# Performance work log

Measured on AMD Instinct MI355X. Metric: run time of the kernel, lower is better.

## Reference

```python
import jax, jax.numpy as jnp
import numpy as np

D_MODEL, D_FF, N_EXPERTS, TOP_K = 1024, 4096, 8, 2

def setup_inputs() -> dict:
    key = jax.random.key(0)
    k0, k1, k2, k3 = jax.random.split(key, 4)
    x = jax.random.normal(k0, (2, 2048, D_MODEL), dtype=jnp.float32)
    Wg = jax.random.normal(k1, (D_MODEL, N_EXPERTS), dtype=jnp.float32) * 0.02
    W1 = jax.random.normal(k2, (N_EXPERTS, D_MODEL, D_FF), dtype=jnp.float32) * 0.02
    b1 = jnp.zeros((N_EXPERTS, D_FF), dtype=jnp.float32)
    W2 = jax.random.normal(k3, (N_EXPERTS, D_FF, D_MODEL), dtype=jnp.float32) * 0.02
    b2 = jnp.zeros((N_EXPERTS, D_MODEL), dtype=jnp.float32)
    return {"x": x, "Wg": Wg, "W1": W1, "b1": b1, "W2": W2, "b2": b2}

def reference(x, Wg, W1, b1, W2, b2):
    B = x.shape[:-1]
    xs = x.reshape(-1, x.shape[-1])                 # [T, D]
    T = xs.shape[0]
    gate_logits = xs @ Wg                           # [T, E]
    weights, sel = jax.lax.top_k(gate_logits, TOP_K)  # [T, k]
    # softmax over the top-k logits, computed in fp32 then cast back (matches F.softmax(dtype=float).type_as)
    weights = jax.nn.softmax(weights.astype(jnp.float32), axis=1).astype(x.dtype)
    # dense all-experts MLP: [E, T, D_FF] -> [E, T, D]
    h = jax.nn.relu(jnp.einsum('td,edf->etf', xs, W1) + b1[:, None, :])
    out_e = jnp.einsum('etf,efd->etd', h, W2) + b2[:, None, :]
    # gather each token's top-k expert outputs and combine with routing weights
    tok = jnp.arange(T)
    picked = out_e[sel, tok[:, None]]               # [T, k, D]
    out = jnp.einsum('tk,tkd->td', weights, picked) # [T, D]
    return out.reshape(*B, x.shape[-1])
```

## Files before the change

### kernel.cpp

```cpp
#include <hip/hip_runtime.h>
#include <cstdint>
#include <cstddef>

#define T_TOKENS 4096
#define DM 1024
#define DF 4096
#define NE 8
#define TOPK 2
#define BK 32
#define MAX_MT 72

typedef short short8 __attribute__((ext_vector_type(8)));
typedef float f32x4 __attribute__((ext_vector_type(4)));

__device__ __forceinline__ unsigned short f2h_bits(float f) {
  _Float16 h = (_Float16)f;
  union { _Float16 h; unsigned short u; } v; v.h = h; return v.u;
}

typedef __attribute__((address_space(3))) void lds_void_t;
typedef __attribute__((address_space(1))) void gvoid_t;
__device__ __forceinline__ void gl_lds16(const void* g, void* l) {
  __builtin_amdgcn_global_load_lds((gvoid_t*)g, (lds_void_t*)l, 16, 0, 0);
}

__global__ void gate_kernel(const float* __restrict__ x, const float* __restrict__ Wg,
                            int* __restrict__ sel, float* __restrict__ wts,
                            int* __restrict__ counts) {
  int wave = threadIdx.x >> 6, lane = threadIdx.x & 63;
  int t = blockIdx.x * 4 + wave;
  const float* xr = x + (size_t)t * DM;
  float acc[NE];
#pragma unroll
  for (int e = 0; e < NE; e++) acc[e] = 0.f;
#pragma unroll
  for (int j = 0; j < DM / 64; j++) {
    int d = lane + 64 * j;
    float xv = xr[d];
    const float* wr = Wg + (size_t)d * NE;
#pragma unroll
    for (int e = 0; e < NE; e++) acc[e] += xv * wr[e];
  }
#pragma unroll
  for (int e = 0; e < NE; e++) {
    float v = acc[e];
#pragma unroll
    for (int off = 32; off > 0; off >>= 1) v += __shfl_down(v, off, 64);
    acc[e] = v;
  }
  if (lane == 0) {
    int b0 = 0;
#pragma unroll
    for (int e = 1; e < NE; e++) if (acc[e] > acc[b0]) b0 = e;
    int b1 = (b0 == 0) ? 1 : 0;
#pragma unroll
    for (int e = 0; e < NE; e++) if (e != b0 && acc[e] > acc[b1]) b1 = e;
    float p = expf(acc[b1] - acc[b0]);
    float w0 = 1.f / (1.f + p);
    sel[t * 2] = b0; sel[t * 2 + 1] = b1;
    wts[t * 2] = w0; wts[t * 2 + 1] = p * w0;
    atomicAdd(&counts[b0], 1);
    atomicAdd(&counts[b1], 1);
  }
}

__global__ void scan_kernel(const int* __restrict__ counts, int* __restrict__ offsets,
                            int* __restrict__ tile_off, int* __restrict__ cursors) {
  if (threadIdx.x == 0) {
    int o = 0, to = 0;
    offsets[0] = 0; tile_off[0] = 0;
    for (int e = 0; e < NE; e++) {
      cursors[e] = o;
      o += counts[e];
      to += (counts[e] + 127) >> 7;
      offsets[e + 1] = o;
      tile_off[e + 1] = to;
    }
  }
}

__global__ void scatter_kernel(const int* __restrict__ sel, const float* __restrict__ wts,
                               int* __restrict__ cursors, int* __restrict__ rows,
                               float* __restrict__ rw) {
  int t = blockIdx.x * 256 + threadIdx.x;
  if (t >= T_TOKENS) return;
#pragma unroll
  for (int k = 0; k < TOPK; k++) {
    int e = sel[t * 2 + k];
    int slot = atomicAdd(&cursors[e], 1);
    rows[slot] = t;
    rw[slot] = wts[t * 2 + k];
  }
}

__global__ void gather_kernel(const float* __restrict__ x, const int* __restrict__ rows,
                              unsigned short* __restrict__ Xg) {
  int wave = threadIdx.x >> 6, lane = threadIdx.x & 63;
  int s = blockIdx.x * 4 + wave;
  int t = rows[s];
  const float4* src = (const float4*)(x + (size_t)t * DM);
  ushort4* dst = (ushort4*)(Xg + (size_t)s * DM);
#pragma unroll
  for (int j = 0; j < 4; j++) {
    float4 v = src[lane + 64 * j];
    ushort4 o;
    o.x = f2h_bits(v.x); o.y = f2h_bits(v.y); o.z = f2h_bits(v.z); o.w = f2h_bits(v.w);
    dst[lane + 64 * j] = o;
  }
}

__global__ void transpose_convert(const float* __restrict__ in, unsigned short* __restrict__ outp,
                                  int R, int C) {
  __shared__ float tile[32][33];
  const float* inE = in + (size_t)blockIdx.z * R * C;
  unsigned short* outE = outp + (size_t)blockIdx.z * R * C;
  int c0 = blockIdx.x * 32, r0 = blockIdx.y * 32;
  int tx = threadIdx.x, ty = threadIdx.y;
#pragma unroll
  for (int k = 0; k < 4; k++)
    tile[ty + 8 * k][tx] = inE[(size_t)(r0 + ty + 8 * k) * C + c0 + tx];
  __syncthreads();
#pragma unroll
  for (int k = 0; k < 4; k++)
    outE[(size_t)(c0 + ty + 8 * k) * R + r0 + tx] = f2h_bits(tile[tx][ty + 8 * k]);
}

template <int K, int N, bool SECOND>
__global__ __launch_bounds__(256, 2) void moe_gemm(
    const unsigned short* __restrict__ Aall, const unsigned short* __restrict__ Ball,
    unsigned short* __restrict__ Hout, float* __restrict__ out,
    const float* __restrict__ bias, const int* __restrict__ counts,
    const int* __restrict__ offsets, const int* __restrict__ tile_off,
    const int* __restrict__ rows, const float* __restrict__ rw) {
  __shared__ __align__(16) unsigned short ldsA[128 * BK];
  __shared__ __align__(16) unsigned short ldsB[128 * BK];

  int bx = blockIdx.x;
  int e = 0;
#pragma unroll 1
  while (e < NE && bx >= tile_off[e + 1]) e++;
  if (e >= NE) return;
  int lt = bx - tile_off[e];
  int cnt = counts[e];
  int m0 = lt * 128;
  int rowbase = offsets[e];
  int n0 = blockIdx.y * 128;

  const unsigned short* Ae = Aall + (size_t)rowbase * K;
  const unsigned short* Be = Ball + ((size_t)e * N + n0) * K;

  int tid = threadIdx.x;
  int lane = tid & 63, wave = tid >> 6;
  int wm = wave & 1, wn = wave >> 1;

  int rA0 = tid >> 2, rA1 = (256 + tid) >> 2, seg = tid & 3;
  int gA0 = m0 + rA0; if (gA0 >= cnt) gA0 = cnt - 1;
  int gA1 = m0 + rA1; if (gA1 >= cnt) gA1 = cnt - 1;
  const unsigned short* srcA0 = Ae + (size_t)gA0 * K + seg * 8;
  const unsigned short* srcA1 = Ae + (size_t)gA1 * K + seg * 8;
  const unsigned short* srcB0 = Be + (size_t)rA0 * K + seg * 8;
  const unsigned short* srcB1 = Be + (size_t)rA1 * K + seg * 8;
  unsigned short* dA0 = ldsA + (size_t)tid * 8;
  unsigned short* dA1 = ldsA + (size_t)(256 + tid) * 8;
  unsigned short* dB0 = ldsB + (size_t)tid * 8;
  unsigned short* dB1 = ldsB + (size_t)(256 + tid) * 8;

  f32x4 acc[4][4] = {};

  for (int kk = 0; kk < K; kk += BK) {
    gl_lds16(srcA0 + kk, dA0);
    gl_lds16(srcA1 + kk, dA1);
    gl_lds16(srcB0 + kk, dB0);
    gl_lds16(srcB1 + kk, dB1);
    __syncthreads();

    short8 af[4], bfr[4];
#pragma unroll
    for (int t4 = 0; t4 < 4; t4++) {
      af[t4]  = *(const short8*)(ldsA + (wm * 64 + t4 * 16 + (lane & 15)) * BK + (lane >> 4) * 8);
      bfr[t4] = *(const short8*)(ldsB + (wn * 64 + t4 * 16 + (lane & 15)) * BK + (lane >> 4) * 8);
    }
#pragma unroll
    for (int tm = 0; tm < 4; tm++)
#pragma unroll
      for (int tn = 0; tn < 4; tn++)
        acc[tm][tn] = __builtin_amdgcn_mfma_f32_16x16x32_f16(af[tm], bfr[tn], acc[tm][tn], 0, 0, 0);
    __syncthreads();
  }

  int quad = lane >> 4, c16 = lane & 15;
#pragma unroll
  for (int tm = 0; tm < 4; tm++) {
#pragma unroll
    for (int tn = 0; tn < 4; tn++) {
      int gcol = n0 + wn * 64 + tn * 16 + c16;
      float b = bias[e * N + gcol];
#pragma unroll
      for (int r = 0; r < 4; r++) {
        int rl = wm * 64 + tm * 16 + quad * 4 + r;
        if (m0 + rl < cnt) {
          float v = acc[tm][tn][r] + b;
          if constexpr (!SECOND) {
            v = fmaxf(v, 0.f);
            Hout[(size_t)(rowbase + m0 + rl) * N + gcol] = f2h_bits(v);
          } else {
            int slot = rowbase + m0 + rl;
            atomicAdd(out + (size_t)rows[slot] * N + gcol, v * rw[slot]);
          }
        }
      }
    }
  }
}

extern "C" void kernel_launch(void* const* d_in, const int* in_sizes, int n_in,
                              void* d_out, int out_size, void* d_ws, size_t ws_size,
                              hipStream_t stream) {
  const float* x  = (const float*)d_in[0];
  const float* Wg = (const float*)d_in[1];
  const float* W1 = (const float*)d_in[2];
  const float* b1 = (const float*)d_in[3];
  const float* W2 = (const float*)d_in[4];
  const float* b2 = (const float*)d_in[5];
  float* out = (float*)d_out;

  char* ws = (char*)d_ws;
  int*   counts   = (int*)(ws + 0);
  int*   cursors  = (int*)(ws + 64);
  int*   offsets  = (int*)(ws + 128);
  int*   tile_off = (int*)(ws + 192);
  int*   sel      = (int*)(ws + 256);
  float* wts      = (float*)(ws + 33024);
  int*   rows     = (int*)(ws + 65792);
  float* rw       = (float*)(ws + 98560);
  unsigned short* Xg  = (unsigned short*)(ws + 131328);
  unsigned short* H   = (unsigned short*)(ws + 131328 + 16777216);
  unsigned short* W1t = (unsigned short*)(ws + 131328 + 16777216 + 67108864);
  unsigned short* W2t = (unsigned short*)(ws + 131328 + 16777216 + 2 * 67108864);

  hipMemsetAsync(ws, 0, 256, stream);
  hipMemsetAsync(d_out, 0, (size_t)out_size * sizeof(float), stream);

  gate_kernel<<<T_TOKENS / 4, 256, 0, stream>>>(x, Wg, sel, wts, counts);
  scan_kernel<<<1, 64, 0, stream>>>(counts, offsets, tile_off, cursors);
  scatter_kernel<<<T_TOKENS / 256, 256, 0, stream>>>(sel, wts, cursors, rows, rw);
  gather_kernel<<<(TOPK * T_TOKENS) / 4, 256, 0, stream>>>(x, rows, Xg);
  transpose_convert<<<dim3(DF / 32, DM / 32, NE), dim3(32, 8), 0, stream>>>(W1, W1t, DM, DF);
  transpose_convert<<<dim3(DM / 32, DF / 32, NE), dim3(32, 8), 0, stream>>>(W2, W2t, DF, DM);

  moe_gemm<DM, DF, false><<<dim3(MAX_MT, DF / 128), 256, 0, stream>>>(
      Xg, W1t, H, out, b1, counts, offsets, tile_off, rows, rw);
  moe_gemm<DF, DM, true><<<dim3(MAX_MT, DM / 128), 256, 0, stream>>>(
      H, W2t, nullptr, out, b2, counts, offsets, tile_off, rows, rw);
}
```

Before: 754.1 us.

## Replace gather and atomic combine with indirect A loads, staged stores, deterministic combine

The gate kernel now writes an fp16 copy of x, and the first GEMM reads rows through the token index, which removes the separate gather kernel. The weight transpose switches to 64x64 tiles with float4 loads and 16-byte fp16 stores. The first GEMM stages its ReLU output through LDS so H is written with wide coalesced stores. The second GEMM writes weighted per-slot results to a scratch buffer, and a new combine kernel sums each token's two slots, replacing fp32 atomics and the output memset. The cost is an extra fp32 scratch buffer, reusing the W1t region, plus one more kernel launch.

```diff
diff --git a/kernel.cpp b/kernel.cpp
--- a/kernel.cpp
+++ b/kernel.cpp
@@ -26,10 +26,11 @@
 
 __global__ void gate_kernel(const float* __restrict__ x, const float* __restrict__ Wg,
                             int* __restrict__ sel, float* __restrict__ wts,
-                            int* __restrict__ counts) {
+                            int* __restrict__ counts, unsigned short* __restrict__ Xh) {
   int wave = threadIdx.x >> 6, lane = threadIdx.x & 63;
   int t = blockIdx.x * 4 + wave;
   const float* xr = x + (size_t)t * DM;
+  unsigned short* xh = Xh + (size_t)t * DM;
   float acc[NE];
 #pragma unroll
   for (int e = 0; e < NE; e++) acc[e] = 0.f;
@@ -37,6 +38,7 @@
   for (int j = 0; j < DM / 64; j++) {
     int d = lane + 64 * j;
     float xv = xr[d];
+    xh[d] = f2h_bits(xv);
     const float* wr = Wg + (size_t)d * NE;
 #pragma unroll
     for (int e = 0; e < NE; e++) acc[e] += xv * wr[e];
@@ -81,7 +83,7 @@
 
 __global__ void scatter_kernel(const int* __restrict__ sel, const float* __restrict__ wts,
                                int* __restrict__ cursors, int* __restrict__ rows,
-                               float* __restrict__ rw) {
+                               float* __restrict__ rw, int* __restrict__ inv) {
   int t = blockIdx.x * 256 + threadIdx.x;
   if (t >= T_TOKENS) return;
 #pragma unroll
@@ -90,50 +92,47 @@
     int slot = atomicAdd(&cursors[e], 1);
     rows[slot] = t;
     rw[slot] = wts[t * 2 + k];
-  }
-}
-
-__global__ void gather_kernel(const float* __restrict__ x, const int* __restrict__ rows,
-                              unsigned short* __restrict__ Xg) {
-  int wave = threadIdx.x >> 6, lane = threadIdx.x & 63;
-  int s = blockIdx.x * 4 + wave;
-  int t = rows[s];
-  const float4* src = (const float4*)(x + (size_t)t * DM);
-  ushort4* dst = (ushort4*)(Xg + (size_t)s * DM);
-#pragma unroll
-  for (int j = 0; j < 4; j++) {
-    float4 v = src[lane + 64 * j];
-    ushort4 o;
-    o.x = f2h_bits(v.x); o.y = f2h_bits(v.y); o.z = f2h_bits(v.z); o.w = f2h_bits(v.w);
-    dst[lane + 64 * j] = o;
+    inv[t * 2 + k] = slot;
   }
 }
 
 __global__ void transpose_convert(const float* __restrict__ in, unsigned short* __restrict__ outp,
                                   int R, int C) {
-  __shared__ float tile[32][33];
+  __shared__ unsigned short ldsT[64 * 72];
   const float* inE = in + (size_t)blockIdx.z * R * C;
   unsigned short* outE = outp + (size_t)blockIdx.z * R * C;
-  int c0 = blockIdx.x * 32, r0 = blockIdx.y * 32;
-  int tx = threadIdx.x, ty = threadIdx.y;
-#pragma unroll
-  for (int k = 0; k < 4; k++)
-    tile[ty + 8 * k][tx] = inE[(size_t)(r0 + ty + 8 * k) * C + c0 + tx];
+  int c0 = blockIdx.x * 64, r0 = blockIdx.y * 64;
+  int tid = threadIdx.x;
+  int rr = tid >> 4, cc4 = (tid & 15) * 4;
+#pragma unroll
+  for (int it = 0; it < 4; it++) {
+    int r = rr + 16 * it;
+    float4 v = *(const float4*)(inE + (size_t)(r0 + r) * C + c0 + cc4);
+    ldsT[(cc4 + 0) * 72 + r] = f2h_bits(v.x);
+    ldsT[(cc4 + 1) * 72 + r] = f2h_bits(v.y);
+    ldsT[(cc4 + 2) * 72 + r] = f2h_bits(v.z);
+    ldsT[(cc4 + 3) * 72 + r] = f2h_bits(v.w);
+  }
   __syncthreads();
 #pragma unroll
-  for (int k = 0; k < 4; k++)
-    outE[(size_t)(c0 + ty + 8 * k) * R + r0 + tx] = f2h_bits(tile[tx][ty + 8 * k]);
-}
-
-template <int K, int N, bool SECOND>
+  for (int it = 0; it < 2; it++) {
+    int idx = tid + 256 * it;
+    int c = idx >> 3, r8 = (idx & 7) * 8;
+    short8 val = *(const short8*)(ldsT + c * 72 + r8);
+    *(short8*)(outE + (size_t)(c0 + c) * R + r0 + r8) = val;
+  }
+}
+
+template <int K, int N, bool INDIR, bool SECOND>
 __global__ __launch_bounds__(256, 2) void moe_gemm(
     const unsigned short* __restrict__ Aall, const unsigned short* __restrict__ Ball,
-    unsigned short* __restrict__ Hout, float* __restrict__ out,
+    unsigned short* __restrict__ Hout, float* __restrict__ Sout,
     const float* __restrict__ bias, const int* __restrict__ counts,
     const int* __restrict__ offsets, const int* __restrict__ tile_off,
     const int* __restrict__ rows, const float* __restrict__ rw) {
-  __shared__ __align__(16) unsigned short ldsA[128 * BK];
-  __shared__ __align__(16) unsigned short ldsB[128 * BK];
+  __shared__ __align__(16) unsigned short lds[8704];
+  unsigned short* ldsA = lds;
+  unsigned short* ldsB = lds + 4096;
 
   int bx = blockIdx.x;
   int e = 0;
@@ -146,7 +145,6 @@
   int rowbase = offsets[e];
   int n0 = blockIdx.y * 128;
 
-  const unsigned short* Ae = Aall + (size_t)rowbase * K;
   const unsigned short* Be = Ball + ((size_t)e * N + n0) * K;
 
   int tid = threadIdx.x;
@@ -154,10 +152,12 @@
   int wm = wave & 1, wn = wave >> 1;
 
   int rA0 = tid >> 2, rA1 = (256 + tid) >> 2, seg = tid & 3;
-  int gA0 = m0 + rA0; if (gA0 >= cnt) gA0 = cnt - 1;
-  int gA1 = m0 + rA1; if (gA1 >= cnt) gA1 = cnt - 1;
-  const unsigned short* srcA0 = Ae + (size_t)gA0 * K + seg * 8;
-  const unsigned short* srcA1 = Ae + (size_t)gA1 * K + seg * 8;
+  int mA0 = m0 + rA0; if (mA0 >= cnt) mA0 = cnt - 1;
+  int mA1 = m0 + rA1; if (mA1 >= cnt) mA1 = cnt - 1;
+  size_t ia0 = INDIR ? (size_t)rows[rowbase + mA0] : (size_t)(rowbase + mA0);
+  size_t ia1 = INDIR ? (size_t)rows[rowbase + mA1] : (size_t)(rowbase + mA1);
+  const unsigned short* srcA0 = Aall + ia0 * K + seg * 8;
+  const unsigned short* srcA1 = Aall + ia1 * K + seg * 8;
   const unsigned short* srcB0 = Be + (size_t)rA0 * K + seg * 8;
   const unsigned short* srcB1 = Be + (size_t)rA1 * K + seg * 8;
   unsigned short* dA0 = ldsA + (size_t)tid * 8;
@@ -189,27 +189,71 @@
   }
 
   int quad = lane >> 4, c16 = lane & 15;
-#pragma unroll
-  for (int tm = 0; tm < 4; tm++) {
-#pragma unroll
-    for (int tn = 0; tn < 4; tn++) {
-      int gcol = n0 + wn * 64 + tn * 16 + c16;
-      float b = bias[e * N + gcol];
-#pragma unroll
-      for (int r = 0; r < 4; r++) {
-        int rl = wm * 64 + tm * 16 + quad * 4 + r;
-        if (m0 + rl < cnt) {
-          float v = acc[tm][tn][r] + b;
-          if constexpr (!SECOND) {
-            v = fmaxf(v, 0.f);
-            Hout[(size_t)(rowbase + m0 + rl) * N + gcol] = f2h_bits(v);
-          } else {
+  if constexpr (!SECOND) {
+#pragma unroll 1
+    for (int half = 0; half < 2; half++) {
+      __syncthreads();
+      if (wm == half) {
+#pragma unroll
+        for (int tm = 0; tm < 4; tm++) {
+#pragma unroll
+          for (int tn = 0; tn < 4; tn++) {
+            int colL = wn * 64 + tn * 16 + c16;
+            float b = bias[e * N + n0 + colL];
+#pragma unroll
+            for (int r = 0; r < 4; r++) {
+              int rl = tm * 16 + quad * 4 + r;
+              float v = fmaxf(acc[tm][tn][r] + b, 0.f);
+              lds[rl * 136 + colL] = f2h_bits(v);
+            }
+          }
+        }
+      }
+      __syncthreads();
+#pragma unroll
+      for (int i = 0; i < 4; i++) {
+        int idx = tid + 256 * i;
+        int row = idx >> 4, c8 = (idx & 15) * 8;
+        int grow = m0 + half * 64 + row;
+        if (grow < cnt) {
+          short8 val = *(const short8*)(lds + row * 136 + c8);
+          *(short8*)(Hout + (size_t)(rowbase + grow) * N + n0 + c8) = val;
+        }
+      }
+    }
+  } else {
+#pragma unroll
+    for (int tm = 0; tm < 4; tm++) {
+#pragma unroll
+      for (int tn = 0; tn < 4; tn++) {
+        int gcol = n0 + wn * 64 + tn * 16 + c16;
+        float b = bias[e * N + gcol];
+#pragma unroll
+        for (int r = 0; r < 4; r++) {
+          int rl = wm * 64 + tm * 16 + quad * 4 + r;
+          if (m0 + rl < cnt) {
             int slot = rowbase + m0 + rl;
-            atomicAdd(out + (size_t)rows[slot] * N + gcol, v * rw[slot]);
+            Sout[(size_t)slot * N + gcol] = (acc[tm][tn][r] + b) * rw[slot];
           }
         }
       }
     }
+  }
+}
+
+__global__ void combine_kernel(const float* __restrict__ S, const int* __restrict__ inv,
+                               float* __restrict__ out) {
+  int wave = threadIdx.x >> 6, lane = threadIdx.x & 63;
+  int t = blockIdx.x * 4 + wave;
+  int s0 = inv[t * 2], s1 = inv[t * 2 + 1];
+  const float4* a = (const float4*)(S + (size_t)s0 * DM);
+  const float4* b = (const float4*)(S + (size_t)s1 * DM);
+  float4* o = (float4*)(out + (size_t)t * DM);
+#pragma unroll
+  for (int j = 0; j < 4; j++) {
+    float4 va = a[lane + 64 * j], vb = b[lane + 64 * j];
+    float4 vo; vo.x = va.x + vb.x; vo.y = va.y + vb.y; vo.z = va.z + vb.z; vo.w = va.w + vb.w;
+    o[lane + 64 * j] = vo;
   }
 }
 
@@ -233,23 +277,25 @@
   float* wts      = (float*)(ws + 33024);
   int*   rows     = (int*)(ws + 65792);
   float* rw       = (float*)(ws + 98560);
-  unsigned short* Xg  = (unsigned short*)(ws + 131328);
-  unsigned short* H   = (unsigned short*)(ws + 131328 + 16777216);
-  unsigned short* W1t = (unsigned short*)(ws + 131328 + 16777216 + 67108864);
-  unsigned short* W2t = (unsigned short*)(ws + 131328 + 16777216 + 2 * 67108864);
-
-  hipMemsetAsync(ws, 0, 256, stream);
-  hipMemsetAsync(d_out, 0, (size_t)out_size * sizeof(float), stream);
-
-  gate_kernel<<<T_TOKENS / 4, 256, 0, stream>>>(x, Wg, sel, wts, counts);
+  int*   inv      = (int*)(ws + 131328);
+  unsigned short* Xh  = (unsigned short*)(ws + 164096);
+  unsigned short* H   = (unsigned short*)(ws + 8552704);
+  unsigned short* W1t = (unsigned short*)(ws + 75661568);
+  float*          S   = (float*)(ws + 75661568);
+  unsigned short* W2t = (unsigned short*)(ws + 142770432);
+
+  hipMemsetAsync(ws, 0, 128, stream);
+
+  gate_kernel<<<T_TOKENS / 4, 256, 0, stream>>>(x, Wg, sel, wts, counts, Xh);
   scan_kernel<<<1, 64, 0, stream>>>(counts, offsets, tile_off, cursors);
-  scatter_kernel<<<T_TOKENS / 256, 256, 0, stream>>>(sel, wts, cursors, rows, rw);
-  gather_kernel<<<(TOPK * T_TOKENS) / 4, 256, 0, stream>>>(x, rows, Xg);
-  transpose_convert<<<dim3(DF / 32, DM / 32, NE), dim3(32, 8), 0, stream>>>(W1, W1t, DM, DF);
-  transpose_convert<<<dim3(DM / 32, DF / 32, NE), dim3(32, 8), 0, stream>>>(W2, W2t, DF, DM);
-
-  moe_gemm<DM, DF, false><<<dim3(MAX_MT, DF / 128), 256, 0, stream>>>(
-      Xg, W1t, H, out, b1, counts, offsets, tile_off, rows, rw);
-  moe_gemm<DF, DM, true><<<dim3(MAX_MT, DM / 128), 256, 0, stream>>>(
-      H, W2t, nullptr, out, b2, counts, offsets, tile_off, rows, rw);
-}
+  scatter_kernel<<<T_TOKENS / 256, 256, 0, stream>>>(sel, wts, cursors, rows, rw, inv);
+  transpose_convert<<<dim3(DF / 64, DM / 64, NE), 256, 0, stream>>>(W1, W1t, DM, DF);
+  transpose_convert<<<dim3(DM / 64, DF / 64, NE), 256, 0, stream>>>(W2, W2t, DF, DM);
+
+  moe_gemm<DM, DF, true, false><<<dim3(MAX_MT, DF / 128), 256, 0, stream>>>(
+      Xh, W1t, H, nullptr, b1, counts, offsets, tile_off, rows, rw);
+  moe_gemm<DF, DM, false, true><<<dim3(MAX_MT, DM / 128), 256, 0, stream>>>(
+      H, W2t, nullptr, S, b2, counts, offsets, tile_off, rows, rw);
+
+  combine_kernel<<<T_TOKENS / 4, 256, 0, stream>>>(S, inv, out);
+}
```

Measured after the change: 713.6 us. -5.4%, faster.
